# Optimization experiments

Hardware: AMD Instinct MI355X
Metric: run time of the kernel (lower is better)

The kernel has to match this reference:

```python
import jax, jax.numpy as jnp
import numpy as np

FEATURE_DIM = 128
N_NODES = 100000
N_EDGES = 800000
L1_IN = 2 * FEATURE_DIM            # 256
L1_OUT = int((2 * FEATURE_DIM) ** 0.5)  # 16
L2_DIM = L1_OUT + 1                # 17


def leaky(x):
    return jnp.where(x >= 0, x, 0.1 * x)


def setup_inputs() -> dict:
    key = jax.random.key(0)
    ks = jax.random.split(key, 8)
    Jt_ind = jax.random.randint(ks[0], (2, N_EDGES), 0, N_NODES)
    Jt_val = jax.random.normal(ks[1], (N_EDGES,), dtype=jnp.float32)
    f = jax.random.normal(ks[2], (N_NODES, FEATURE_DIM), dtype=jnp.float32)
    W1 = jax.random.normal(ks[3], (L1_IN, L1_OUT), dtype=jnp.float32) * (1.0 / np.sqrt(L1_IN))
    b1 = jnp.zeros((L1_OUT,), dtype=jnp.float32)
    W2 = jax.random.normal(ks[4], (L2_DIM, L2_DIM), dtype=jnp.float32) * (1.0 / np.sqrt(L2_DIM))
    b2 = jnp.zeros((L2_DIM,), dtype=jnp.float32)
    Wc = jax.random.normal(ks[5], (L2_DIM, 1), dtype=jnp.float32) * (1.0 / np.sqrt(L2_DIM))
    bc = jnp.ones((1,), dtype=jnp.float32)  # collapse_bias = 1
    return {"Jt_ind": Jt_ind, "Jt_val": Jt_val, "f": f, "N": N_NODES,
            "W1": W1, "b1": b1, "W2": W2, "b2": b2, "Wc": Wc, "bc": bc}


def reference(Jt_ind, Jt_val, f, N, W1, b1, W2, b2, Wc, bc):
    i = Jt_ind[0]
    j = Jt_ind[1]
    absv = jnp.abs(Jt_val)                                     # [E]
    # degree: per-destination sum of |Jt_val|
    deg_abs = jax.ops.segment_sum(absv, i, num_segments=N)     # [N]
    Jt_val_abs_norm = absv / deg_abs[i]                        # [E]
    # gather endpoint features and run tiny edge-MLP
    x = jnp.concatenate([f[i], f[j]], axis=1)                  # [E, 2F]
    x = leaky(x @ W1 + b1)                                     # [E, L1_OUT]
    x = jnp.concatenate([x, Jt_val_abs_norm[:, None]], axis=1) # [E, L2_DIM]
    x = leaky(x @ W2 + b2)                                     # [E, L2_DIM]
    e_values = (x @ Wc + bc)[:, 0]                             # [E]
    # segment softmax over edges grouped by destination i (stable)
    m = jax.ops.segment_max(e_values, i, num_segments=N)       # [N]
    ex = jnp.exp(e_values - m[i])                              # [E]
    s = jax.ops.segment_sum(ex, i, num_segments=N)             # [N]
    return ex / s[i]                                           # [E]
```

## Files before the change

kernel.cpp:

```cpp
#include <hip/hip_runtime.h>
#include <hip/hip_fp16.h>
#include <math.h>

#define FDIM  128
#define L1OUT 16
#define L2DIM 17
#define TRM   128
#define HSTR  136
#define WSTR  136

typedef _Float16 f16x8 __attribute__((ext_vector_type(8)));
typedef float    f32x4 __attribute__((ext_vector_type(4)));

struct __align__(16) H16 { __half2 h[8]; };

__device__ __forceinline__ float lrelu(float v) { return v >= 0.f ? v : 0.1f * v; }

__global__ void node_transform(
    const float* __restrict__ f, const float* __restrict__ W1,
    const float* __restrict__ b1,
    const int* __restrict__ ind_i, const float* __restrict__ val,
    H16* __restrict__ A, H16* __restrict__ B,
    float* __restrict__ deg, int N, int E)
{
    __shared__ __align__(16) _Float16 tile[TRM * HSTR];
    __shared__ __align__(16) _Float16 w1t[32 * WSTR];

    const int t    = threadIdx.x;
    const int gtid = blockIdx.x * 256 + t;
    const int GT   = gridDim.x * 256;

    {
        const int E4 = E >> 2;
        for (int q = gtid; q < E4; q += GT) {
            int e = q << 2;
            int4   ii = *reinterpret_cast<const int4*>(ind_i + e);
            float4 vv = *reinterpret_cast<const float4*>(val + e);
            atomicAdd(&deg[ii.x], fabsf(vv.x));
            atomicAdd(&deg[ii.y], fabsf(vv.y));
            atomicAdd(&deg[ii.z], fabsf(vv.z));
            atomicAdd(&deg[ii.w], fabsf(vv.w));
        }
        if (gtid < (E & 3)) {
            int e = (E & ~3) + gtid;
            atomicAdd(&deg[ind_i[e]], fabsf(val[e]));
        }
    }

    {
#pragma unroll
        for (int q = 0; q < 4; ++q) {
            int i4 = t + 256 * q;
            float4 v = reinterpret_cast<const float4*>(W1)[i4];
            int k  = i4 >> 2;
            int n0 = (i4 & 3) * 4;
            int nn = (k >= FDIM) ? 16 : 0;
            int kk = k & (FDIM - 1);
            w1t[(nn + n0 + 0) * WSTR + kk] = (_Float16)v.x;
            w1t[(nn + n0 + 1) * WSTR + kk] = (_Float16)v.y;
            w1t[(nn + n0 + 2) * WSTR + kk] = (_Float16)v.z;
            w1t[(nn + n0 + 3) * WSTR + kk] = (_Float16)v.w;
        }
    }

    const int base = blockIdx.x * TRM;
#pragma unroll
    for (int q = 0; q < 8; ++q) {
        int p  = t + 256 * q;
        int r  = p >> 4;
        int c8 = p & 15;
        float4 lo = make_float4(0.f, 0.f, 0.f, 0.f);
        float4 hi = lo;
        if (base + r < N) {
            const float4* src = reinterpret_cast<const float4*>(
                f + (size_t)(base + r) * FDIM + c8 * 8);
            lo = src[0];
            hi = src[1];
        }
        f16x8 hx;
        hx[0] = (_Float16)lo.x; hx[1] = (_Float16)lo.y;
        hx[2] = (_Float16)lo.z; hx[3] = (_Float16)lo.w;
        hx[4] = (_Float16)hi.x; hx[5] = (_Float16)hi.y;
        hx[6] = (_Float16)hi.z; hx[7] = (_Float16)hi.w;
        *reinterpret_cast<f16x8*>(&tile[r * HSTR + c8 * 8]) = hx;
    }
    __syncthreads();

    const int lane = t & 63;
    const int wv   = t >> 6;
    const int n    = lane & 15;
    const int quad = lane >> 4;

    f16x8 bfr[2][4];
#pragma unroll
    for (int nt = 0; nt < 2; ++nt)
#pragma unroll
        for (int ks = 0; ks < 4; ++ks)
            bfr[nt][ks] = *reinterpret_cast<const f16x8*>(
                &w1t[(nt * 16 + n) * WSTR + 32 * ks + 8 * quad]);
    float b1v = b1[n];

#pragma unroll
    for (int si = 0; si < 2; ++si) {
        const int m0 = (wv + 4 * si) * 16;
        f32x4 acc0 = { b1v, b1v, b1v, b1v };
        f32x4 acc1 = { 0.f, 0.f, 0.f, 0.f };
#pragma unroll
        for (int ks = 0; ks < 4; ++ks) {
            f16x8 af = *reinterpret_cast<const f16x8*>(
                &tile[(m0 + n) * HSTR + 32 * ks + 8 * quad]);
            acc0 = __builtin_amdgcn_mfma_f32_16x16x32_f16(af, bfr[0][ks], acc0, 0, 0, 0);
            acc1 = __builtin_amdgcn_mfma_f32_16x16x32_f16(af, bfr[1][ks], acc1, 0, 0, 0);
        }
#pragma unroll
        for (int reg = 0; reg < 4; ++reg) {
            int node = base + m0 + quad * 4 + reg;
            if (node < N) {
                reinterpret_cast<_Float16*>(A + node)[n] = (_Float16)acc0[reg];
                reinterpret_cast<_Float16*>(B + node)[n] = (_Float16)acc1[reg];
            }
        }
    }
}

__global__ void edge_mlp(
    const int* __restrict__ ind, const float* __restrict__ val,
    const H16* __restrict__ A, const H16* __restrict__ B,
    const float* __restrict__ deg,
    const float* __restrict__ W2, const float* __restrict__ b2,
    const float* __restrict__ Wc, const float* __restrict__ bc,
    float* __restrict__ eout, float* __restrict__ ssum, int E)
{
    __shared__ float w2s[L2DIM * 20];
    __shared__ float b2s[L2DIM];
    __shared__ float wcs[L2DIM];
    __shared__ float bc0s;

    const int t = threadIdx.x;
    for (int idx = t; idx < L2DIM * L2DIM; idx += 256) {
        int c = idx / L2DIM, r = idx - c * L2DIM;
        w2s[c * 20 + r] = W2[idx];
    }
    if (t < L2DIM) b2s[t] = b2[t];
    if (t < L2DIM) wcs[t] = Wc[t];
    if (t == 0)    bc0s   = bc[0];
    __syncthreads();

    const int e = blockIdx.x * 256 + t;
    if (e >= E) return;

    int   i = ind[e];
    int   j = ind[E + e];
    H16   a  = A[i];
    H16   bb = B[j];
    float v  = val[e];
    float dg = deg[i];

    float x[L2DIM];
#pragma unroll
    for (int q = 0; q < 8; ++q) {
        float2 fa = __half22float2(a.h[q]);
        float2 fb = __half22float2(bb.h[q]);
        x[2 * q]     = lrelu(fa.x + fb.x);
        x[2 * q + 1] = lrelu(fa.y + fb.y);
    }
    x[L1OUT] = fabsf(v) / dg;

    float acc[L2DIM];
#pragma unroll
    for (int r = 0; r < L2DIM; ++r) acc[r] = b2s[r];
#pragma unroll
    for (int c = 0; c < L2DIM; ++c) {
        float xc = x[c];
        const float4* r4 = reinterpret_cast<const float4*>(&w2s[c * 20]);
        float4 w0 = r4[0], w1v = r4[1], w2v = r4[2], w3 = r4[3];
        float  w16 = w2s[c * 20 + 16];
        acc[0]  += xc * w0.x;  acc[1]  += xc * w0.y;
        acc[2]  += xc * w0.z;  acc[3]  += xc * w0.w;
        acc[4]  += xc * w1v.x; acc[5]  += xc * w1v.y;
        acc[6]  += xc * w1v.z; acc[7]  += xc * w1v.w;
        acc[8]  += xc * w2v.x; acc[9]  += xc * w2v.y;
        acc[10] += xc * w2v.z; acc[11] += xc * w2v.w;
        acc[12] += xc * w3.x;  acc[13] += xc * w3.y;
        acc[14] += xc * w3.z;  acc[15] += xc * w3.w;
        acc[16] += xc * w16;
    }
    float ev = bc0s;
#pragma unroll
    for (int r = 0; r < L2DIM; ++r) ev += lrelu(acc[r]) * wcs[r];

    float ex = __expf(ev);
    eout[e] = ex;
    atomicAdd(&ssum[i], ex);
}

__global__ void normalize(const int* __restrict__ ind_i, const float* __restrict__ ssum,
                          float* __restrict__ ex, int E) {
    int t = blockIdx.x * blockDim.x + threadIdx.x;
    int e = t * 4;
    if (e + 3 < E) {
        int4   ii = *reinterpret_cast<const int4*>(ind_i + e);
        float4 vv = *reinterpret_cast<const float4*>(ex + e);
        vv.x /= ssum[ii.x];
        vv.y /= ssum[ii.y];
        vv.z /= ssum[ii.z];
        vv.w /= ssum[ii.w];
        *reinterpret_cast<float4*>(ex + e) = vv;
    } else {
        for (; e < E; ++e) ex[e] = ex[e] / ssum[ind_i[e]];
    }
}

extern "C" void kernel_launch(void* const* d_in, const int* in_sizes, int n_in,
                              void* d_out, int out_size, void* d_ws, size_t ws_size,
                              hipStream_t stream) {
    const int*   Jt_ind = (const int*)  d_in[0];
    const float* Jt_val = (const float*)d_in[1];
    const float* f      = (const float*)d_in[2];
    const float* W1 = (const float*)d_in[4];
    const float* b1 = (const float*)d_in[5];
    const float* W2 = (const float*)d_in[6];
    const float* b2 = (const float*)d_in[7];
    const float* Wc = (const float*)d_in[8];
    const float* bc = (const float*)d_in[9];

    const int E = in_sizes[1];
    const int N = in_sizes[2] / FDIM;
    float* out = (float*)d_out;

    char* ws = (char*)d_ws;
    float* deg  = (float*)ws;  ws += (size_t)N * sizeof(float);
    float* ssum = (float*)ws;  ws += (size_t)N * sizeof(float);
    H16*   A    = (H16*)ws;    ws += (size_t)N * sizeof(H16);
    H16*   Bm   = (H16*)ws;    ws += (size_t)N * sizeof(H16);

    const int B256 = 256;
    const int nblk = (N + TRM - 1) / TRM;
    const int eblk = (E + B256 - 1) / B256;
    const int qblk = ((E + 3) / 4 + B256 - 1) / B256;

    hipMemsetAsync(deg, 0, 2 * (size_t)N * sizeof(float), stream);
    node_transform<<<nblk, B256, 0, stream>>>(f, W1, b1, Jt_ind, Jt_val,
                                              A, Bm, deg, N, E);
    edge_mlp      <<<eblk, B256, 0, stream>>>(Jt_ind, Jt_val, A, Bm, deg,
                                              W2, b2, Wc, bc, out, ssum, E);
    normalize     <<<qblk, B256, 0, stream>>>(Jt_ind, ssum, out, E);
}
```

Before: 211.9 us.

## Process two edges per thread in edge MLP and halve node tile size

The edge MLP kernel now handles two consecutive edges per thread, using paired int2/float2 loads for indices and values, a float2 store for outputs, and launch bounds of 256 threads with 4 blocks. The node transform tile shrinks from 128 to 64 rows, doubling its block count, which also spreads the degree atomics over more blocks. The intent is to expose more memory-level parallelism for the random gathers and to improve occupancy in the node kernel. In exchange each edge-MLP thread uses more registers and there are half as many edge threads.

```diff
diff --git a/kernel.cpp b/kernel.cpp
--- a/kernel.cpp
+++ b/kernel.cpp
@@ -5,14 +5,13 @@
 #define FDIM  128
 #define L1OUT 16
 #define L2DIM 17
-#define TRM   128
+#define TRM   64
 #define HSTR  136
 #define WSTR  136
 
-typedef _Float16 f16x8 __attribute__((ext_vector_type(8)));
-typedef float    f32x4 __attribute__((ext_vector_type(4)));
-
-struct __align__(16) H16 { __half2 h[8]; };
+typedef _Float16 f16x8  __attribute__((ext_vector_type(8)));
+typedef _Float16 f16x16 __attribute__((ext_vector_type(16)));
+typedef float    f32x4  __attribute__((ext_vector_type(4)));
 
 __device__ __forceinline__ float lrelu(float v) { return v >= 0.f ? v : 0.1f * v; }
 
@@ -20,7 +19,7 @@
     const float* __restrict__ f, const float* __restrict__ W1,
     const float* __restrict__ b1,
     const int* __restrict__ ind_i, const float* __restrict__ val,
-    H16* __restrict__ A, H16* __restrict__ B,
+    _Float16* __restrict__ A, _Float16* __restrict__ B,
     float* __restrict__ deg, int N, int E)
 {
     __shared__ __align__(16) _Float16 tile[TRM * HSTR];
@@ -65,7 +64,7 @@
 
     const int base = blockIdx.x * TRM;
 #pragma unroll
-    for (int q = 0; q < 8; ++q) {
+    for (int q = 0; q < 4; ++q) {
         int p  = t + 256 * q;
         int r  = p >> 4;
         int c8 = p & 15;
@@ -90,6 +89,7 @@
     const int wv   = t >> 6;
     const int n    = lane & 15;
     const int quad = lane >> 4;
+    const int m0   = wv * 16;
 
     f16x8 bfr[2][4];
 #pragma unroll
@@ -100,32 +100,28 @@
                 &w1t[(nt * 16 + n) * WSTR + 32 * ks + 8 * quad]);
     float b1v = b1[n];
 
-#pragma unroll
-    for (int si = 0; si < 2; ++si) {
-        const int m0 = (wv + 4 * si) * 16;
-        f32x4 acc0 = { b1v, b1v, b1v, b1v };
-        f32x4 acc1 = { 0.f, 0.f, 0.f, 0.f };
-#pragma unroll
-        for (int ks = 0; ks < 4; ++ks) {
-            f16x8 af = *reinterpret_cast<const f16x8*>(
-                &tile[(m0 + n) * HSTR + 32 * ks + 8 * quad]);
-            acc0 = __builtin_amdgcn_mfma_f32_16x16x32_f16(af, bfr[0][ks], acc0, 0, 0, 0);
-            acc1 = __builtin_amdgcn_mfma_f32_16x16x32_f16(af, bfr[1][ks], acc1, 0, 0, 0);
-        }
-#pragma unroll
-        for (int reg = 0; reg < 4; ++reg) {
-            int node = base + m0 + quad * 4 + reg;
-            if (node < N) {
-                reinterpret_cast<_Float16*>(A + node)[n] = (_Float16)acc0[reg];
-                reinterpret_cast<_Float16*>(B + node)[n] = (_Float16)acc1[reg];
-            }
-        }
-    }
-}
-
-__global__ void edge_mlp(
+    f32x4 acc0 = { b1v, b1v, b1v, b1v };
+    f32x4 acc1 = { 0.f, 0.f, 0.f, 0.f };
+#pragma unroll
+    for (int ks = 0; ks < 4; ++ks) {
+        f16x8 af = *reinterpret_cast<const f16x8*>(
+            &tile[(m0 + n) * HSTR + 32 * ks + 8 * quad]);
+        acc0 = __builtin_amdgcn_mfma_f32_16x16x32_f16(af, bfr[0][ks], acc0, 0, 0, 0);
+        acc1 = __builtin_amdgcn_mfma_f32_16x16x32_f16(af, bfr[1][ks], acc1, 0, 0, 0);
+    }
+#pragma unroll
+    for (int reg = 0; reg < 4; ++reg) {
+        int node = base + m0 + quad * 4 + reg;
+        if (node < N) {
+            A[(size_t)node * L1OUT + n] = (_Float16)acc0[reg];
+            B[(size_t)node * L1OUT + n] = (_Float16)acc1[reg];
+        }
+    }
+}
+
+__global__ __launch_bounds__(256, 4) void edge_mlp(
     const int* __restrict__ ind, const float* __restrict__ val,
-    const H16* __restrict__ A, const H16* __restrict__ B,
+    const _Float16* __restrict__ A, const _Float16* __restrict__ B,
     const float* __restrict__ deg,
     const float* __restrict__ W2, const float* __restrict__ b2,
     const float* __restrict__ Wc, const float* __restrict__ bc,
@@ -146,52 +142,90 @@
     if (t == 0)    bc0s   = bc[0];
     __syncthreads();
 
-    const int e = blockIdx.x * 256 + t;
-    if (e >= E) return;
-
-    int   i = ind[e];
-    int   j = ind[E + e];
-    H16   a  = A[i];
-    H16   bb = B[j];
-    float v  = val[e];
-    float dg = deg[i];
-
-    float x[L2DIM];
-#pragma unroll
-    for (int q = 0; q < 8; ++q) {
-        float2 fa = __half22float2(a.h[q]);
-        float2 fb = __half22float2(bb.h[q]);
-        x[2 * q]     = lrelu(fa.x + fb.x);
-        x[2 * q + 1] = lrelu(fa.y + fb.y);
-    }
-    x[L1OUT] = fabsf(v) / dg;
-
-    float acc[L2DIM];
-#pragma unroll
-    for (int r = 0; r < L2DIM; ++r) acc[r] = b2s[r];
+    const int e0 = (blockIdx.x * 256 + t) * 2;
+    if (e0 >= E) return;
+    const bool has1 = (e0 + 1) < E;
+
+    int2   ii = *reinterpret_cast<const int2*>(ind + e0);
+    int2   jj = *reinterpret_cast<const int2*>(ind + E + e0);
+    float2 vv = *reinterpret_cast<const float2*>(val + e0);
+    int i0 = ii.x, i1 = has1 ? ii.y : ii.x;
+    int j0 = jj.x, j1 = has1 ? jj.y : jj.x;
+
+    f16x16 a0 = *reinterpret_cast<const f16x16*>(A + (size_t)i0 * L1OUT);
+    f16x16 g0 = *reinterpret_cast<const f16x16*>(B + (size_t)j0 * L1OUT);
+    f16x16 a1 = *reinterpret_cast<const f16x16*>(A + (size_t)i1 * L1OUT);
+    f16x16 g1 = *reinterpret_cast<const f16x16*>(B + (size_t)j1 * L1OUT);
+    float  d0 = deg[i0];
+    float  d1 = deg[i1];
+
+    float x0[L2DIM];
+#pragma unroll
+    for (int c = 0; c < L1OUT; ++c)
+        x0[c] = lrelu((float)a0[c] + (float)g0[c]);
+    x0[L1OUT] = fabsf(vv.x) / d0;
+
+    float acc0[L2DIM];
+#pragma unroll
+    for (int r = 0; r < L2DIM; ++r) acc0[r] = b2s[r];
 #pragma unroll
     for (int c = 0; c < L2DIM; ++c) {
-        float xc = x[c];
+        float xc = x0[c];
         const float4* r4 = reinterpret_cast<const float4*>(&w2s[c * 20]);
         float4 w0 = r4[0], w1v = r4[1], w2v = r4[2], w3 = r4[3];
         float  w16 = w2s[c * 20 + 16];
-        acc[0]  += xc * w0.x;  acc[1]  += xc * w0.y;
-        acc[2]  += xc * w0.z;  acc[3]  += xc * w0.w;
-        acc[4]  += xc * w1v.x; acc[5]  += xc * w1v.y;
-        acc[6]  += xc * w1v.z; acc[7]  += xc * w1v.w;
-        acc[8]  += xc * w2v.x; acc[9]  += xc * w2v.y;
-        acc[10] += xc * w2v.z; acc[11] += xc * w2v.w;
-        acc[12] += xc * w3.x;  acc[13] += xc * w3.y;
-        acc[14] += xc * w3.z;  acc[15] += xc * w3.w;
-        acc[16] += xc * w16;
-    }
-    float ev = bc0s;
-#pragma unroll
-    for (int r = 0; r < L2DIM; ++r) ev += lrelu(acc[r]) * wcs[r];
-
-    float ex = __expf(ev);
-    eout[e] = ex;
-    atomicAdd(&ssum[i], ex);
+        acc0[0]  += xc * w0.x;  acc0[1]  += xc * w0.y;
+        acc0[2]  += xc * w0.z;  acc0[3]  += xc * w0.w;
+        acc0[4]  += xc * w1v.x; acc0[5]  += xc * w1v.y;
+        acc0[6]  += xc * w1v.z; acc0[7]  += xc * w1v.w;
+        acc0[8]  += xc * w2v.x; acc0[9]  += xc * w2v.y;
+        acc0[10] += xc * w2v.z; acc0[11] += xc * w2v.w;
+        acc0[12] += xc * w3.x;  acc0[13] += xc * w3.y;
+        acc0[14] += xc * w3.z;  acc0[15] += xc * w3.w;
+        acc0[16] += xc * w16;
+    }
+    float ev0 = bc0s;
+#pragma unroll
+    for (int r = 0; r < L2DIM; ++r) ev0 += lrelu(acc0[r]) * wcs[r];
+    float ex0 = __expf(ev0);
+
+    float x1[L2DIM];
+#pragma unroll
+    for (int c = 0; c < L1OUT; ++c)
+        x1[c] = lrelu((float)a1[c] + (float)g1[c]);
+    x1[L1OUT] = fabsf(vv.y) / d1;
+
+    float acc1[L2DIM];
+#pragma unroll
+    for (int r = 0; r < L2DIM; ++r) acc1[r] = b2s[r];
+#pragma unroll
+    for (int c = 0; c < L2DIM; ++c) {
+        float xc = x1[c];
+        const float4* r4 = reinterpret_cast<const float4*>(&w2s[c * 20]);
+        float4 w0 = r4[0], w1v = r4[1], w2v = r4[2], w3 = r4[3];
+        float  w16 = w2s[c * 20 + 16];
+        acc1[0]  += xc * w0.x;  acc1[1]  += xc * w0.y;
+        acc1[2]  += xc * w0.z;  acc1[3]  += xc * w0.w;
+        acc1[4]  += xc * w1v.x; acc1[5]  += xc * w1v.y;
+        acc1[6]  += xc * w1v.z; acc1[7]  += xc * w1v.w;
+        acc1[8]  += xc * w2v.x; acc1[9]  += xc * w2v.y;
+        acc1[10] += xc * w2v.z; acc1[11] += xc * w2v.w;
+        acc1[12] += xc * w3.x;  acc1[13] += xc * w3.y;
+        acc1[14] += xc * w3.z;  acc1[15] += xc * w3.w;
+        acc1[16] += xc * w16;
+    }
+    float ev1 = bc0s;
+#pragma unroll
+    for (int r = 0; r < L2DIM; ++r) ev1 += lrelu(acc1[r]) * wcs[r];
+    float ex1 = __expf(ev1);
+
+    atomicAdd(&ssum[i0], ex0);
+    if (has1) {
+        atomicAdd(&ssum[i1], ex1);
+        *reinterpret_cast<float2*>(eout + e0) = make_float2(ex0, ex1);
+    } else {
+        eout[e0] = ex0;
+    }
 }
 
 __global__ void normalize(const int* __restrict__ ind_i, const float* __restrict__ ssum,
@@ -229,14 +263,14 @@
     float* out = (float*)d_out;
 
     char* ws = (char*)d_ws;
-    float* deg  = (float*)ws;  ws += (size_t)N * sizeof(float);
-    float* ssum = (float*)ws;  ws += (size_t)N * sizeof(float);
-    H16*   A    = (H16*)ws;    ws += (size_t)N * sizeof(H16);
-    H16*   Bm   = (H16*)ws;    ws += (size_t)N * sizeof(H16);
+    float*    deg  = (float*)ws;     ws += (size_t)N * sizeof(float);
+    float*    ssum = (float*)ws;     ws += (size_t)N * sizeof(float);
+    _Float16* A    = (_Float16*)ws;  ws += (size_t)N * L1OUT * sizeof(_Float16);
+    _Float16* Bm   = (_Float16*)ws;  ws += (size_t)N * L1OUT * sizeof(_Float16);
 
     const int B256 = 256;
     const int nblk = (N + TRM - 1) / TRM;
-    const int eblk = (E + B256 - 1) / B256;
+    const int eblk = ((E + 1) / 2 + B256 - 1) / B256;
     const int qblk = ((E + 3) / 4 + B256 - 1) / B256;
 
     hipMemsetAsync(deg, 0, 2 * (size_t)N * sizeof(float), stream);
```

Result: slower. 443.3 us (+109.2%).
